# Optimization experiments

Hardware: AMD Instinct MI355X
Metric: run time of the kernel (lower is better)

Reference implementation:

```python
import jax, jax.numpy as jnp
import numpy as np

DIM = 4096
NH = 32
NKV = 8
HD = DIM // NH          # 128
REP = NH // NKV          # 4
B = 1
T = 2048
THETA = 500000.0
NEG = -1e9


def setup_inputs() -> dict:
    key = jax.random.key(0)
    ks = jax.random.split(key, 6)
    x = jax.random.normal(ks[0], (B, T, DIM), jnp.float32)
    # RoPE tables (real/imag parts of freqs_cis = exp(i * t * inv_freq))
    inv_freq = 1.0 / (THETA ** (np.arange(0, HD, 2, dtype=np.float32) / HD))  # (HD/2,)
    ang = np.outer(np.arange(T, dtype=np.float32), inv_freq)                  # (T, HD/2)
    freqs_cos = jnp.asarray(np.cos(ang), jnp.float32)
    freqs_sin = jnp.asarray(np.sin(ang), jnp.float32)
    # additive causal mask for prefill (pos=0): (T, T)
    mask = jnp.where(np.tril(np.ones((T, T), dtype=bool)), 0.0, NEG).astype(jnp.float32)
    cache_k = jnp.zeros((B, T, NKV, HD), jnp.float32)
    cache_v = jnp.zeros((B, T, NKV, HD), jnp.float32)
    s = 0.02
    wk_w = jax.random.normal(ks[1], (NKV * HD, DIM), jnp.float32) * s
    wk_b = jnp.zeros((NKV * HD,), jnp.float32)
    wv_w = jax.random.normal(ks[2], (NKV * HD, DIM), jnp.float32) * s
    wv_b = jnp.zeros((NKV * HD,), jnp.float32)
    wo_w = jax.random.normal(ks[3], (DIM, DIM), jnp.float32) * s
    wo_b = jnp.zeros((DIM,), jnp.float32)
    return dict(x=x, freqs_cos=freqs_cos, freqs_sin=freqs_sin, mask=mask,
                cache_k=cache_k, cache_v=cache_v,
                wk_w=wk_w, wk_b=wk_b, wv_w=wv_w, wv_b=wv_b,
                wo_w=wo_w, wo_b=wo_b, pos=0)


def _rope(t, cos, sin):
    # t: (B, T, H, HD); pairs (even, odd) form complex numbers
    tr = t.reshape(*t.shape[:-1], HD // 2, 2)
    re, im = tr[..., 0], tr[..., 1]
    c = cos[None, :, None, :]
    s = sin[None, :, None, :]
    out = jnp.stack([re * c - im * s, re * s + im * c], axis=-1)
    return out.reshape(t.shape)


def reference(x, freqs_cos, freqs_sin, mask, cache_k, cache_v,
              wk_w, wk_b, wv_w, wv_b, wo_w, wo_b, pos):
    Bx, Tx, D = x.shape
    # NOTE: faithful to source bug -- q projection uses wo (shared with output proj)
    q = x @ wo_w.T + wo_b                        # (B, T, D)
    k = x @ wk_w.T + wk_b                        # (B, T, NKV*HD)
    v = x @ wv_w.T + wv_b
    q = q.reshape(Bx, Tx, NH, HD)
    k = k.reshape(Bx, Tx, NKV, HD)
    v = v.reshape(Bx, Tx, NKV, HD)
    q = _rope(q, freqs_cos, freqs_sin)
    k = _rope(k, freqs_cos, freqs_sin)
    # KV-cache append then read back [:pos+T]
    ck = cache_k.at[:Bx, pos:pos + Tx].set(k)
    cv = cache_v.at[:Bx, pos:pos + Tx].set(v)
    k = ck[:Bx, :pos + Tx]
    v = cv[:Bx, :pos + Tx]
    # repeat_kv (GQA expansion)
    k = jnp.repeat(k, REP, axis=2)               # (B, S, NH, HD)
    v = jnp.repeat(v, REP, axis=2)
    scale = 1.0 / jnp.sqrt(jnp.float32(HD))
    scores = jnp.einsum('bqhd,bkhd->bhqk', q, k) * scale
    scores = scores + mask[None, None, :, :]
    p = jax.nn.softmax(scores.astype(jnp.float32), axis=-1)
    out = jnp.einsum('bhqk,bkhd->bqhd', p, v).reshape(Bx, Tx, D)
    return out @ wo_w.T + wo_b
```

## Files before the change

### kernel.cpp

```cpp
#include <hip/hip_runtime.h>
#include <stdint.h>
#include <stddef.h>

#define T_SEQ 2048
#define DIM   4096
#define NH    32
#define NKV   8
#define HD    128
#define KVD   (NKV*HD)

typedef __attribute__((ext_vector_type(8))) short short8;
typedef __attribute__((ext_vector_type(4))) float floatx4;

static __device__ __forceinline__ float bf2f(short u) {
    union { unsigned int i; float f; } c; c.i = ((unsigned int)(unsigned short)u) << 16; return c.f;
}
static __device__ __forceinline__ short f2bf(float f) {
    union { float f; unsigned int u; } c; c.f = f;
    unsigned int r = c.u + 0x7fff + ((c.u >> 16) & 1);
    return (short)(r >> 16);
}
static __device__ __forceinline__ short8 ld8_f2b(const float* p) {
    floatx4 a = *(const floatx4*)p;
    floatx4 b = *(const floatx4*)(p + 4);
    short8 r;
    r[0]=f2bf(a[0]); r[1]=f2bf(a[1]); r[2]=f2bf(a[2]); r[3]=f2bf(a[3]);
    r[4]=f2bf(b[0]); r[5]=f2bf(b[1]); r[6]=f2bf(b[2]); r[7]=f2bf(b[3]);
    return r;
}

#define GLD16(g, l) __builtin_amdgcn_global_load_lds( \
    (const __attribute__((address_space(1))) unsigned int*)(g), \
    (__attribute__((address_space(3))) unsigned int*)(l), 16, 0, 0)

template<int CTRL>
static __device__ __forceinline__ float dppf(float x) {
    return __int_as_float(__builtin_amdgcn_update_dpp(
        0, __float_as_int(x), CTRL, 0xf, 0xf, true));
}
static __device__ __forceinline__ float rowmax16(float x) {
    x = fmaxf(x, dppf<0xB1>(x));
    x = fmaxf(x, dppf<0x4E>(x));
    x = fmaxf(x, dppf<0x141>(x));
    x = fmaxf(x, dppf<0x140>(x));
    return x;
}
static __device__ __forceinline__ float rowsum16(float x) {
    x += dppf<0xB1>(x);
    x += dppf<0x4E>(x);
    x += dppf<0x141>(x);
    x += dppf<0x140>(x);
    return x;
}

__global__ __launch_bounds__(256)
void cvt_bf16(const float* __restrict__ x, const float* __restrict__ wk,
              const float* __restrict__ wv, const float* __restrict__ wo,
              short* __restrict__ xb, short* __restrict__ wkb,
              short* __restrict__ wvb, short* __restrict__ wob) {
    size_t i8 = ((size_t)blockIdx.x * 256 + threadIdx.x) * 8;
    const float* src; short* dst; size_t off;
    if (i8 < 8388608)        { src = x;  dst = xb;  off = i8; }
    else if (i8 < 12582912)  { src = wk; dst = wkb; off = i8 - 8388608; }
    else if (i8 < 16777216)  { src = wv; dst = wvb; off = i8 - 12582912; }
    else                     { src = wo; dst = wob; off = i8 - 16777216; }
    *(short8*)(dst + off) = ld8_f2b(src + off);
}

template<bool C_F32>
static __device__ __forceinline__
void gemm_core(const short* __restrict__ A, const short* __restrict__ B,
               const float* __restrict__ bias, void* __restrict__ Cp,
               int N, int K, int bm, int bn) {
    __shared__ short sA0[128*32];
    __shared__ short sA1[128*32];
    __shared__ short sB0[128*32];
    __shared__ short sB1[128*32];
    const int tid  = threadIdx.x;
    const int wave = tid >> 6, lane = tid & 63;
    const int l15  = lane & 15, lq = lane >> 4;
    const int wm   = (wave >> 1) * 64, wn = (wave & 1) * 64;

    floatx4 acc[4][4];
    #pragma unroll
    for (int i = 0; i < 4; i++)
        #pragma unroll
        for (int j = 0; j < 4; j++)
            acc[i][j] = (floatx4)(0.0f);

    const int c0 = tid, c1 = 256 + tid;
    const int r0 = c0 >> 2, k0 = (c0 & 3) * 8;
    const int r1 = c1 >> 2, k1 = (c1 & 3) * 8;
    const short* pA0 = A + (size_t)(bm + r0) * K + k0;
    const short* pA1 = A + (size_t)(bm + r1) * K + k1;
    const short* pB0 = B + (size_t)(bn + r0) * K + k0;
    const short* pB1 = B + (size_t)(bn + r1) * K + k1;

    auto stage = [&](short* dA, short* dB, int kt) {
        GLD16(pA0 + kt, dA + c0 * 8);
        GLD16(pA1 + kt, dA + c1 * 8);
        GLD16(pB0 + kt, dB + c0 * 8);
        GLD16(pB1 + kt, dB + c1 * 8);
    };
    auto compute = [&](const short* dA, const short* dB) {
        short8 af[4], bfr[4];
        #pragma unroll
        for (int mi = 0; mi < 4; mi++)
            af[mi] = *(const short8*)&dA[(wm + mi*16 + l15)*32 + lq*8];
        #pragma unroll
        for (int ni = 0; ni < 4; ni++)
            bfr[ni] = *(const short8*)&dB[(wn + ni*16 + l15)*32 + lq*8];
        #pragma unroll
        for (int mi = 0; mi < 4; mi++)
            #pragma unroll
            for (int ni = 0; ni < 4; ni++)
                acc[mi][ni] = __builtin_amdgcn_mfma_f32_16x16x32_bf16(af[mi], bfr[ni], acc[mi][ni], 0, 0, 0);
    };

    stage(sA0, sB0, 0);
    __syncthreads();

    const int nt = K >> 5;
    for (int t = 0; t < nt; t += 2) {
        stage(sA1, sB1, (t + 1) * 32);
        compute(sA0, sB0);
        __syncthreads();
        if (t + 2 < nt) stage(sA0, sB0, (t + 2) * 32);
        compute(sA1, sB1);
        __syncthreads();
    }

    #pragma unroll
    for (int ni = 0; ni < 4; ni++) {
        int col = bn + wn + ni*16 + l15;
        float bv = bias[col];
        #pragma unroll
        for (int mi = 0; mi < 4; mi++) {
            int row = bm + wm + mi*16 + lq*4;
            #pragma unroll
            for (int r = 0; r < 4; r++) {
                float v = acc[mi][ni][r] + bv;
                if (C_F32) ((float*)Cp)[(size_t)(row + r)*N + col] = v;
                else       ((short*)Cp)[(size_t)(row + r)*N + col] = f2bf(v);
            }
        }
    }
}

template<bool C_F32>
__global__ __launch_bounds__(256)
void gemm_bt(const short* __restrict__ A, const short* __restrict__ B,
             const float* __restrict__ bias, void* __restrict__ Cp,
             int N, int K) {
    gemm_core<C_F32>(A, B, bias, Cp, N, K, blockIdx.y * 128, blockIdx.x * 128);
}

__global__ __launch_bounds__(256)
void gemm_kv(const short* __restrict__ A,
             const short* __restrict__ Bk, const float* __restrict__ bk, short* __restrict__ Ck,
             const short* __restrict__ Bv, const float* __restrict__ bv, short* __restrict__ Cv) {
    const short* B = blockIdx.z ? Bv : Bk;
    const float* bias = blockIdx.z ? bv : bk;
    short* C = blockIdx.z ? Cv : Ck;
    gemm_core<false>(A, B, bias, C, KVD, DIM, blockIdx.y * 128, blockIdx.x * 128);
}

#define QSC (0.08838834764831845f * 1.4426950408889634f)

__global__ __launch_bounds__(256)
void rope_k(short* __restrict__ Q, short* __restrict__ Kc,
            const float* __restrict__ fc, const float* __restrict__ fs) {
    int idx = blockIdx.x * 256 + threadIdx.x;
    const int NQ = T_SEQ * NH  * (HD/2);
    const int NK = T_SEQ * NKV * (HD/2);
    short* base; int t, i; size_t off; float sc;
    if (idx < NQ) {
        i = idx & 63;
        int th = idx >> 6;
        t = th >> 5;
        off = (size_t)th * HD + i*2;
        base = Q; sc = QSC;
    } else if (idx < NQ + NK) {
        int kidx = idx - NQ;
        i = kidx & 63;
        int th = kidx >> 6;
        t = th >> 3;
        off = (size_t)th * HD + i*2;
        base = Kc; sc = 1.0f;
    } else return;
    float re = bf2f(base[off]), im = bf2f(base[off+1]);
    float c = fc[t*64 + i], s = fs[t*64 + i];
    base[off]   = f2bf((re*c - im*s)*sc);
    base[off+1] = f2bf((re*s + im*c)*sc);
}

__global__ __launch_bounds__(256)
void vtrans(const short* __restrict__ V, short* __restrict__ Vt) {
    __shared__ short sT[64*72];
    const int tid = threadIdx.x;
    const int bt = blockIdx.x, bd = blockIdx.y;
    #pragma unroll
    for (int i = 0; i < 2; i++) {
        int c = i*256 + tid;
        int r = c >> 3, c8 = (c & 7) * 8;
        *(short8*)&sT[r*72 + c8] = *(const short8*)(V + (size_t)(bt*64 + r)*KVD + bd*64 + c8);
    }
    __syncthreads();
    #pragma unroll
    for (int i = 0; i < 2; i++) {
        int c = i*256 + tid;
        int d = c >> 3, t8 = (c & 7) * 8;
        short8 o;
        #pragma unroll
        for (int j = 0; j < 8; j++) o[j] = sT[(t8 + j)*72 + d];
        *(short8*)(Vt + (size_t)(bd*64 + d)*T_SEQ + bt*64 + t8) = o;
    }
}

__global__ __launch_bounds__(256, 2)
void flash_attn(const short* __restrict__ Q, const short* __restrict__ Kc,
                const short* __restrict__ Vt, short* __restrict__ O) {
    __shared__ short sK0[64*128];
    __shared__ short sK1[64*128];
    __shared__ short sV0[128*64];
    __shared__ short sV1[128*64];
    __shared__ short sP[4*2048];
    const int tid  = threadIdx.x;
    const int wave = tid >> 6, lane = tid & 63;
    const int l15  = lane & 15, lq = lane >> 4;
    const int sw   = l15 & 7;
    const int kvg  = blockIdx.y;
    const int qt   = (blockIdx.y < 4) ? (int)blockIdx.x : 63 - (int)blockIdx.x;
    const int hl   = wave;
    const int qb   = qt * 32;

    short8 qf[2][4];
    #pragma unroll
    for (int mi = 0; mi < 2; mi++)
        #pragma unroll
        for (int ks = 0; ks < 4; ks++)
            qf[mi][ks] = *(const short8*)(Q + (size_t)(qb + mi*16 + l15)*DIM
                                          + kvg*512 + hl*128 + ks*32 + lq*8);

    short* sPw = sP + wave*2048;

    int kc_r[4], kc_jg[4], vc_r[4], vc_jg[4];
    #pragma unroll
    for (int i = 0; i < 4; i++) {
        int c = i*256 + tid;
        kc_r[i]  = c >> 4;
        kc_jg[i] = (c & 15) ^ (kc_r[i] & 7);
        vc_r[i]  = c >> 3;
        vc_jg[i] = (c & 7) ^ (vc_r[i] & 7);
    }
    auto stage = [&](short* dK, short* dV, int kt) {
        #pragma unroll
        for (int i = 0; i < 4; i++) {
            int c = i*256 + tid;
            GLD16(Kc + (size_t)(kt*64 + kc_r[i])*KVD + kvg*HD + kc_jg[i]*8,
                  dK + c*8);
            GLD16(Vt + (size_t)(kvg*HD + vc_r[i])*T_SEQ + kt*64 + vc_jg[i]*8,
                  dV + c*8);
        }
    };

    float m_r[2][4], l_r[2][4];
    floatx4 o_acc[2][8];
    #pragma unroll
    for (int mi = 0; mi < 2; mi++) {
        #pragma unroll
        for (int r = 0; r < 4; r++) { m_r[mi][r] = -1e30f; l_r[mi][r] = 0.0f; }
        #pragma unroll
        for (int nd = 0; nd < 8; nd++) o_acc[mi][nd] = (floatx4)(0.0f);
    }

    const int ktmax = qt >> 1;
    stage(sK0, sV0, 0);
    __syncthreads();

    for (int kt = 0; kt <= ktmax; kt++) {
        short* bK = (kt & 1) ? sK1 : sK0;
        short* bV = (kt & 1) ? sV1 : sV0;
        if (kt < ktmax) stage((kt & 1) ? sK0 : sK1, (kt & 1) ? sV0 : sV1, kt + 1);

        floatx4 s_acc[2][4];
        #pragma unroll
        for (int mi = 0; mi < 2; mi++)
            #pragma unroll
            for (int ni = 0; ni < 4; ni++) s_acc[mi][ni] = (floatx4)(0.0f);
        __builtin_amdgcn_s_setprio(1);
        #pragma unroll
        for (int ks = 0; ks < 4; ks++)
            #pragma unroll
            for (int ni = 0; ni < 4; ni++) {
                short8 kf = *(const short8*)&bK[(ni*16 + l15)*128
                                                + (((ks*4 + lq) ^ sw)*8)];
                s_acc[0][ni] = __builtin_amdgcn_mfma_f32_16x16x32_bf16(qf[0][ks], kf, s_acc[0][ni], 0, 0, 0);
                s_acc[1][ni] = __builtin_amdgcn_mfma_f32_16x16x32_bf16(qf[1][ks], kf, s_acc[1][ni], 0, 0, 0);
            }
        __builtin_amdgcn_s_setprio(0);

        const bool last = (kt == ktmax);

        #pragma unroll
        for (int mi = 0; mi < 2; mi++) {
            float sv[4][4], mx[4];
            #pragma unroll
            for (int r = 0; r < 4; r++) mx[r] = -1e30f;
            #pragma unroll
            for (int ni = 0; ni < 4; ni++) {
                int col = kt*64 + ni*16 + l15;
                #pragma unroll
                for (int r = 0; r < 4; r++) {
                    float x = s_acc[mi][ni][r];
                    if (last) {
                        int row = qb + mi*16 + lq*4 + r;
                        x = (col <= row) ? x : -1e30f;
                    }
                    sv[ni][r] = x;
                    mx[r] = fmaxf(mx[r], x);
                }
            }
            #pragma unroll
            for (int r = 0; r < 4; r++) mx[r] = rowmax16(mx[r]);

            float g = fmaxf(fmaxf(mx[0] - m_r[mi][0], mx[1] - m_r[mi][1]),
                            fmaxf(mx[2] - m_r[mi][2], mx[3] - m_r[mi][3]));
            if (__any(g > 8.0f)) {
                #pragma unroll
                for (int r = 0; r < 4; r++) {
                    float mn = fmaxf(m_r[mi][r], mx[r]);
                    float a  = __builtin_amdgcn_exp2f(m_r[mi][r] - mn);
                    m_r[mi][r] = mn;
                    l_r[mi][r] *= a;
                    #pragma unroll
                    for (int nd = 0; nd < 8; nd++) o_acc[mi][nd][r] *= a;
                }
            }

            float rs[4] = {0.0f, 0.0f, 0.0f, 0.0f};
            #pragma unroll
            for (int ni = 0; ni < 4; ni++)
                #pragma unroll
                for (int r = 0; r < 4; r++) {
                    float p = __builtin_amdgcn_exp2f(sv[ni][r] - m_r[mi][r]);
                    sv[ni][r] = p;
                    rs[r] += p;
                }
            #pragma unroll
            for (int r = 0; r < 4; r++) {
                rs[r] = rowsum16(rs[r]);
                l_r[mi][r] += rs[r];
            }

            #pragma unroll
            for (int ni = 0; ni < 4; ni++)
                #pragma unroll
                for (int r = 0; r < 4; r++) {
                    int q = mi*16 + lq*4 + r, k = ni*16 + l15;
                    sPw[q*64 + (((k >> 3) ^ (q & 7))*8) + (k & 7)] = f2bf(sv[ni][r]);
                }
        }

        __builtin_amdgcn_s_setprio(1);
        #pragma unroll
        for (int ks = 0; ks < 2; ks++) {
            int kk = ks*32 + lq*8;
            short8 pf[2];
            #pragma unroll
            for (int mi = 0; mi < 2; mi++) {
                int q = mi*16 + l15;
                pf[mi] = *(const short8*)&sPw[q*64 + (((kk >> 3) ^ (q & 7))*8)];
            }
            #pragma unroll
            for (int nd = 0; nd < 8; nd++) {
                short8 vf = *(const short8*)&bV[(nd*16 + l15)*64
                                                + (((ks*4 + lq) ^ sw)*8)];
                o_acc[0][nd] = __builtin_amdgcn_mfma_f32_16x16x32_bf16(pf[0], vf, o_acc[0][nd], 0, 0, 0);
                o_acc[1][nd] = __builtin_amdgcn_mfma_f32_16x16x32_bf16(pf[1], vf, o_acc[1][nd], 0, 0, 0);
            }
        }
        __builtin_amdgcn_s_setprio(0);

        __syncthreads();
    }

    #pragma unroll
    for (int mi = 0; mi < 2; mi++)
        #pragma unroll
        for (int nd = 0; nd < 8; nd++) {
            int col = (kvg*4 + hl)*HD + nd*16 + l15;
            #pragma unroll
            for (int r = 0; r < 4; r++) {
                int row = qb + mi*16 + lq*4 + r;
                O[(size_t)row*DIM + col] = f2bf(o_acc[mi][nd][r] / l_r[mi][r]);
            }
        }
}

extern "C" void kernel_launch(void* const* d_in, const int* in_sizes, int n_in,
                              void* d_out, int out_size, void* d_ws, size_t ws_size,
                              hipStream_t stream) {
    const float* x    = (const float*)d_in[0];
    const float* fc   = (const float*)d_in[1];
    const float* fs   = (const float*)d_in[2];
    const float* wk_w = (const float*)d_in[6];
    const float* wk_b = (const float*)d_in[7];
    const float* wv_w = (const float*)d_in[8];
    const float* wv_b = (const float*)d_in[9];
    const float* wo_w = (const float*)d_in[10];
    const float* wo_b = (const float*)d_in[11];
    float* out = (float*)d_out;

    short* xb  = (short*)d_ws;
    short* wkb = xb  + 8388608;
    short* wvb = wkb + 4194304;
    short* wob = wvb + 4194304;
    short* Q   = wob + 16777216;
    short* K   = Q   + 8388608;
    short* V   = K   + 2097152;
    short* Vt  = V   + 2097152;
    short* AO  = Vt  + 2097152;

    cvt_bf16<<<dim3(16384), dim3(256), 0, stream>>>(x, wk_w, wv_w, wo_w, xb, wkb, wvb, wob);

    gemm_bt<false><<<dim3(32, 16), dim3(256), 0, stream>>>(xb, wob, wo_b, Q, DIM, DIM);
    gemm_kv<<<dim3(8, 16, 2), dim3(256), 0, stream>>>(xb, wkb, wk_b, K, wvb, wv_b, V);

    int nrope = T_SEQ*NH*(HD/2) + T_SEQ*NKV*(HD/2);
    rope_k<<<dim3((nrope + 255)/256), dim3(256), 0, stream>>>(Q, K, fc, fs);

    vtrans<<<dim3(32, 16), dim3(256), 0, stream>>>(V, Vt);

    flash_attn<<<dim3(64, 8), dim3(256), 0, stream>>>(Q, K, Vt, AO);

    gemm_bt<true><<<dim3(32, 16), dim3(256), 0, stream>>>(AO, wob, wo_b, out, DIM, DIM);
}
```

Before: 519.0 us.

## Transpose QK^T MFMA so each lane owns a query row, simplifying softmax

Swaps the MFMA operands for the score product so S is produced transposed: each lane holds one query row across four key columns. The row max and row sum then need only two cross-lane shuffles instead of per-register DPP reductions, and m/l state drops to one scalar per lane. P is packed with v_cvt_pk_bf16_f32 and written as 8-byte vector stores into swizzled LDS rather than 16 scalar short stores. The rescale factors are broadcast back via shuffles, and the final divide becomes a reciprocal multiply. This adds shuffle traffic inside the rescale branch.

```diff
diff --git a/kernel.cpp b/kernel.cpp
--- a/kernel.cpp
+++ b/kernel.cpp
@@ -11,6 +11,7 @@
 
 typedef __attribute__((ext_vector_type(8))) short short8;
 typedef __attribute__((ext_vector_type(4))) float floatx4;
+typedef __attribute__((ext_vector_type(2))) unsigned int uintx2;
 
 static __device__ __forceinline__ float bf2f(short u) {
     union { unsigned int i; float f; } c; c.i = ((unsigned int)(unsigned short)u) << 16; return c.f;
@@ -32,26 +33,6 @@
 #define GLD16(g, l) __builtin_amdgcn_global_load_lds( \
     (const __attribute__((address_space(1))) unsigned int*)(g), \
     (__attribute__((address_space(3))) unsigned int*)(l), 16, 0, 0)
-
-template<int CTRL>
-static __device__ __forceinline__ float dppf(float x) {
-    return __int_as_float(__builtin_amdgcn_update_dpp(
-        0, __float_as_int(x), CTRL, 0xf, 0xf, true));
-}
-static __device__ __forceinline__ float rowmax16(float x) {
-    x = fmaxf(x, dppf<0xB1>(x));
-    x = fmaxf(x, dppf<0x4E>(x));
-    x = fmaxf(x, dppf<0x141>(x));
-    x = fmaxf(x, dppf<0x140>(x));
-    return x;
-}
-static __device__ __forceinline__ float rowsum16(float x) {
-    x += dppf<0xB1>(x);
-    x += dppf<0x4E>(x);
-    x += dppf<0x141>(x);
-    x += dppf<0x140>(x);
-    return x;
-}
 
 __global__ __launch_bounds__(256)
 void cvt_bf16(const float* __restrict__ x, const float* __restrict__ wk,
@@ -242,7 +223,7 @@
             qf[mi][ks] = *(const short8*)(Q + (size_t)(qb + mi*16 + l15)*DIM
                                           + kvg*512 + hl*128 + ks*32 + lq*8);
 
-    short* sPw = sP + wave*2048;
+    char* pw = (char*)(sP + wave*2048);
 
     int kc_r[4], kc_jg[4], vc_r[4], vc_jg[4];
     #pragma unroll
@@ -264,15 +245,13 @@
         }
     };
 
-    float m_r[2][4], l_r[2][4];
+    float m_r[2] = {-1e30f, -1e30f};
+    float l_r[2] = {0.0f, 0.0f};
     floatx4 o_acc[2][8];
     #pragma unroll
-    for (int mi = 0; mi < 2; mi++) {
-        #pragma unroll
-        for (int r = 0; r < 4; r++) { m_r[mi][r] = -1e30f; l_r[mi][r] = 0.0f; }
+    for (int mi = 0; mi < 2; mi++)
         #pragma unroll
         for (int nd = 0; nd < 8; nd++) o_acc[mi][nd] = (floatx4)(0.0f);
-    }
 
     const int ktmax = qt >> 1;
     stage(sK0, sV0, 0);
@@ -295,8 +274,8 @@
             for (int ni = 0; ni < 4; ni++) {
                 short8 kf = *(const short8*)&bK[(ni*16 + l15)*128
                                                 + (((ks*4 + lq) ^ sw)*8)];
-                s_acc[0][ni] = __builtin_amdgcn_mfma_f32_16x16x32_bf16(qf[0][ks], kf, s_acc[0][ni], 0, 0, 0);
-                s_acc[1][ni] = __builtin_amdgcn_mfma_f32_16x16x32_bf16(qf[1][ks], kf, s_acc[1][ni], 0, 0, 0);
+                s_acc[0][ni] = __builtin_amdgcn_mfma_f32_16x16x32_bf16(kf, qf[0][ks], s_acc[0][ni], 0, 0, 0);
+                s_acc[1][ni] = __builtin_amdgcn_mfma_f32_16x16x32_bf16(kf, qf[1][ks], s_acc[1][ni], 0, 0, 0);
             }
         __builtin_amdgcn_s_setprio(0);
 
@@ -304,74 +283,70 @@
 
         #pragma unroll
         for (int mi = 0; mi < 2; mi++) {
-            float sv[4][4], mx[4];
-            #pragma unroll
-            for (int r = 0; r < 4; r++) mx[r] = -1e30f;
-            #pragma unroll
-            for (int ni = 0; ni < 4; ni++) {
-                int col = kt*64 + ni*16 + l15;
+            float sv[4][4];
+            float mx = -1e30f;
+            const int qrow = qb + mi*16 + l15;
+            #pragma unroll
+            for (int ni = 0; ni < 4; ni++)
                 #pragma unroll
                 for (int r = 0; r < 4; r++) {
                     float x = s_acc[mi][ni][r];
                     if (last) {
-                        int row = qb + mi*16 + lq*4 + r;
-                        x = (col <= row) ? x : -1e30f;
+                        int kcol = kt*64 + ni*16 + lq*4 + r;
+                        x = (kcol <= qrow) ? x : -1e30f;
                     }
                     sv[ni][r] = x;
-                    mx[r] = fmaxf(mx[r], x);
+                    mx = fmaxf(mx, x);
                 }
-            }
-            #pragma unroll
-            for (int r = 0; r < 4; r++) mx[r] = rowmax16(mx[r]);
-
-            float g = fmaxf(fmaxf(mx[0] - m_r[mi][0], mx[1] - m_r[mi][1]),
-                            fmaxf(mx[2] - m_r[mi][2], mx[3] - m_r[mi][3]));
-            if (__any(g > 8.0f)) {
+            mx = fmaxf(mx, __shfl_xor(mx, 16));
+            mx = fmaxf(mx, __shfl_xor(mx, 32));
+
+            if (__any(mx - m_r[mi] > 8.0f)) {
+                float mn = fmaxf(m_r[mi], mx);
+                float a  = __builtin_amdgcn_exp2f(m_r[mi] - mn);
+                m_r[mi] = mn;
+                l_r[mi] *= a;
+                float ar[4];
                 #pragma unroll
-                for (int r = 0; r < 4; r++) {
-                    float mn = fmaxf(m_r[mi][r], mx[r]);
-                    float a  = __builtin_amdgcn_exp2f(m_r[mi][r] - mn);
-                    m_r[mi][r] = mn;
-                    l_r[mi][r] *= a;
+                for (int r = 0; r < 4; r++) ar[r] = __shfl(a, lq*4 + r);
+                #pragma unroll
+                for (int nd = 0; nd < 8; nd++)
                     #pragma unroll
-                    for (int nd = 0; nd < 8; nd++) o_acc[mi][nd][r] *= a;
-                }
-            }
-
-            float rs[4] = {0.0f, 0.0f, 0.0f, 0.0f};
+                    for (int r = 0; r < 4; r++) o_acc[mi][nd][r] *= ar[r];
+            }
+
+            float rs = 0.0f;
             #pragma unroll
             for (int ni = 0; ni < 4; ni++)
                 #pragma unroll
                 for (int r = 0; r < 4; r++) {
-                    float p = __builtin_amdgcn_exp2f(sv[ni][r] - m_r[mi][r]);
+                    float p = __builtin_amdgcn_exp2f(sv[ni][r] - m_r[mi]);
                     sv[ni][r] = p;
-                    rs[r] += p;
+                    rs += p;
                 }
-            #pragma unroll
-            for (int r = 0; r < 4; r++) {
-                rs[r] = rowsum16(rs[r]);
-                l_r[mi][r] += rs[r];
-            }
-
-            #pragma unroll
-            for (int ni = 0; ni < 4; ni++)
-                #pragma unroll
-                for (int r = 0; r < 4; r++) {
-                    int q = mi*16 + lq*4 + r, k = ni*16 + l15;
-                    sPw[q*64 + (((k >> 3) ^ (q & 7))*8) + (k & 7)] = f2bf(sv[ni][r]);
-                }
+            rs += __shfl_xor(rs, 16);
+            rs += __shfl_xor(rs, 32);
+            l_r[mi] += rs;
+
+            char* rowp = pw + (mi*16 + l15)*128 + (lq & 1)*8;
+            #pragma unroll
+            for (int ni = 0; ni < 4; ni++) {
+                unsigned int lo, hi;
+                asm("v_cvt_pk_bf16_f32 %0, %1, %2" : "=v"(lo) : "v"(sv[ni][0]), "v"(sv[ni][1]));
+                asm("v_cvt_pk_bf16_f32 %0, %1, %2" : "=v"(hi) : "v"(sv[ni][2]), "v"(sv[ni][3]));
+                int kc = ni*2 + (lq >> 1);
+                *(uintx2*)(rowp + ((kc ^ sw) * 16)) = (uintx2){lo, hi};
+            }
         }
 
         __builtin_amdgcn_s_setprio(1);
         #pragma unroll
         for (int ks = 0; ks < 2; ks++) {
-            int kk = ks*32 + lq*8;
             short8 pf[2];
             #pragma unroll
-            for (int mi = 0; mi < 2; mi++) {
-                int q = mi*16 + l15;
-                pf[mi] = *(const short8*)&sPw[q*64 + (((kk >> 3) ^ (q & 7))*8)];
-            }
+            for (int mi = 0; mi < 2; mi++)
+                pf[mi] = *(const short8*)(pw + (mi*16 + l15)*128
+                                          + (((ks*4 + lq) ^ sw)*16));
             #pragma unroll
             for (int nd = 0; nd < 8; nd++) {
                 short8 vf = *(const short8*)&bV[(nd*16 + l15)*64
@@ -385,6 +360,13 @@
         __syncthreads();
     }
 
+    float rec[2][4];
+    #pragma unroll
+    for (int mi = 0; mi < 2; mi++) {
+        float rv = 1.0f / l_r[mi];
+        #pragma unroll
+        for (int r = 0; r < 4; r++) rec[mi][r] = __shfl(rv, lq*4 + r);
+    }
     #pragma unroll
     for (int mi = 0; mi < 2; mi++)
         #pragma unroll
@@ -393,7 +375,7 @@
             #pragma unroll
             for (int r = 0; r < 4; r++) {
                 int row = qb + mi*16 + lq*4 + r;
-                O[(size_t)row*DIM + col] = f2bf(o_acc[mi][nd][r] / l_r[mi][r]);
+                O[(size_t)row*DIM + col] = f2bf(o_acc[mi][nd][r] * rec[mi][r]);
             }
         }
 }
```

New measurement: 496.4 us. 4.4% less time.
